# Performance work log

Hardware: AMD Instinct MI355X
Metric: run time of the kernel (lower is better)

The kernel has to match this reference:

```python
import jax, jax.numpy as jnp
import numpy as np


def setup_inputs() -> dict:
    key = jax.random.key(0)
    image = jax.random.randint(key, (4, 2048, 2048), 0, 50000, dtype=jnp.int32)
    return {"image": image}


def reference(image) -> jnp.ndarray:
    # Faithful, single-pass equivalent of LabelGapAdjustment(shift=False).
    # The original while-loop (decrement labels above each missing label until
    # labels are the consecutive set 1..K) is exactly dense-rank remapping:
    # new_label = 1-based rank of the label among the sorted unique labels.
    imin = image.min()
    image_shift = 1 - imin
    shifted = jnp.where(imin <= 0, image + image_shift, image)

    flat = shifted.reshape(-1)
    order = jnp.argsort(flat)
    s = flat[order]  # sorted labels
    # 1 where a new distinct value starts; cumsum -> 1-based dense rank
    is_new = jnp.concatenate(
        [jnp.ones((1,), dtype=jnp.int32), (s[1:] != s[:-1]).astype(jnp.int32)]
    )
    ranks_sorted = jnp.cumsum(is_new)  # [N], values 1..K
    # scatter ranks back to original positions
    ranks = jnp.zeros_like(flat).at[order].set(ranks_sorted.astype(flat.dtype))
    compact = ranks.reshape(image.shape)

    # shift=False: undo the shift (original subtracts image_shift unconditionally)
    return compact - image_shift
```

## Files before the change

### kernel.cpp

```cpp
#include <hip/hip_runtime.h>
#include <limits.h>

#define TABLE 65536
#define NBITW (TABLE / 32)
#define NTAB  512
#define CHUNK 16
#define MIN_OFF 0
#define BITS_OFF 64
#define PACK_OFF (64 + NBITW)
#define TAB_OFF  (PACK_OFF + 2 * NBITW)

__global__ __launch_bounds__(1024) void lga_mark_kernel(const int* __restrict__ img,
                                                        int n, int n4, int* ws) {
    __shared__ unsigned char tbl[TABLE];
    unsigned int* tbl32 = (unsigned int*)tbl;
    int t = threadIdx.x;
    for (int i = t; i < TABLE / 4; i += 1024) tbl32[i] = 0;
    if (blockIdx.x == 0) {
        for (int i = t; i < NBITW; i += 1024) ws[BITS_OFF + i] = 0;
    }
    __syncthreads();

    int stride = gridDim.x * blockDim.x;
    for (int i = blockIdx.x * blockDim.x + t; i < n4; i += stride) {
        int4 v = ((const int4*)img)[i];
        tbl[v.x] = 1;
        tbl[v.y] = 1;
        tbl[v.z] = 1;
        tbl[v.w] = 1;
    }
    if (blockIdx.x == 0 && t == 0) {
        for (int j = n4 * 4; j < n; ++j) tbl[img[j]] = 1;
    }
    __syncthreads();

    unsigned int* mytab = (unsigned int*)(ws + TAB_OFF) + blockIdx.x * NBITW;
    for (int d = t; d < NBITW; d += 1024) {
        const unsigned int* p = tbl32 + d * 8;
        unsigned int m = 0;
        #pragma unroll
        for (int j = 0; j < 8; ++j) {
            unsigned int w = p[j];
            m |= (w & 1u) << (j * 4);
            m |= ((w >> 8) & 1u) << (j * 4 + 1);
            m |= ((w >> 16) & 1u) << (j * 4 + 2);
            m |= ((w >> 24) & 1u) << (j * 4 + 3);
        }
        mytab[d] = m;
    }
}

__global__ __launch_bounds__(128) void lga_merge_kernel(int* ws) {
    int d = blockIdx.x * 128 + threadIdx.x;
    const unsigned int* tabs = (const unsigned int*)(ws + TAB_OFF)
                             + (size_t)blockIdx.y * CHUNK * NBITW;
    unsigned int m = 0;
    #pragma unroll
    for (int k = 0; k < CHUNK; ++k) m |= tabs[k * NBITW + d];
    if (m) atomicOr((unsigned int*)(ws + BITS_OFF) + d, m);
}

__global__ __launch_bounds__(1024) void lga_scan_kernel(int* ws) {
    const unsigned int* bits = (const unsigned int*)(ws + BITS_OFF);
    uint4* pack = (uint4*)(ws + PACK_OFF);
    int t = threadIdx.x;
    int lane = t & 63;
    int wave = t >> 6;

    unsigned int d0 = bits[2 * t], d1 = bits[2 * t + 1];
    int c0 = __popc(d0);
    int s = c0 + __popc(d1);
    int firstset;
    if (d0)      firstset = 64 * t + __ffs(d0) - 1;
    else if (d1) firstset = 64 * t + 32 + __ffs(d1) - 1;
    else         firstset = INT_MAX;

    int v = s;
    #pragma unroll
    for (int off = 1; off < 64; off <<= 1) {
        int u = __shfl_up(v, off, 64);
        if (lane >= off) v += u;
    }
    int fm = firstset;
    #pragma unroll
    for (int off = 32; off > 0; off >>= 1)
        fm = min(fm, __shfl_down(fm, off, 64));

    __shared__ int wsum[16];
    __shared__ int wmin[16];
    if (lane == 63) wsum[wave] = v;
    if (lane == 0)  wmin[wave] = fm;
    __syncthreads();
    if (wave == 0 && lane < 16) {
        int w = wsum[lane];
        #pragma unroll
        for (int off = 1; off < 16; off <<= 1) {
            int u = __shfl_up(w, off, 16);
            if (lane >= off) w += u;
        }
        wsum[lane] = w;
        int m = wmin[lane];
        #pragma unroll
        for (int off = 8; off > 0; off >>= 1)
            m = min(m, __shfl_down(m, off, 16));
        if (lane == 0) ws[MIN_OFF] = m;
    }
    __syncthreads();

    unsigned int excl = (unsigned int)(v - s + (wave > 0 ? wsum[wave - 1] : 0));
    pack[t] = make_uint4(excl, d0, excl + (unsigned int)c0, d1);
}

__global__ __launch_bounds__(1024) void lga_remap_kernel(const int* __restrict__ img,
                                                         int* __restrict__ out,
                                                         int n, int n4,
                                                         const int* __restrict__ ws) {
    __shared__ uint2 lp[NBITW];
    const uint2* pack = (const uint2*)(ws + PACK_OFF);
    int t = threadIdx.x;
    for (int i = t; i < NBITW; i += 1024) lp[i] = pack[i];
    int imin = ws[MIN_OFF];
    __syncthreads();

    int stride = gridDim.x * blockDim.x;
    for (int i = blockIdx.x * blockDim.x + t; i < n4; i += stride) {
        int4 v = ((const int4*)img)[i];
        int4 r;
        {
            uint2 p = lp[((unsigned)v.x) >> 5];
            r.x = (int)(p.x + __popc(p.y & ((1u << (v.x & 31)) - 1u))) + imin;
        }
        {
            uint2 p = lp[((unsigned)v.y) >> 5];
            r.y = (int)(p.x + __popc(p.y & ((1u << (v.y & 31)) - 1u))) + imin;
        }
        {
            uint2 p = lp[((unsigned)v.z) >> 5];
            r.z = (int)(p.x + __popc(p.y & ((1u << (v.z & 31)) - 1u))) + imin;
        }
        {
            uint2 p = lp[((unsigned)v.w) >> 5];
            r.w = (int)(p.x + __popc(p.y & ((1u << (v.w & 31)) - 1u))) + imin;
        }
        ((int4*)out)[i] = r;
    }
    if (blockIdx.x == 0 && t == 0) {
        for (int j = n4 * 4; j < n; ++j) {
            unsigned v = (unsigned)img[j];
            uint2 p = lp[v >> 5];
            out[j] = (int)(p.x + __popc(p.y & ((1u << (v & 31)) - 1u))) + imin;
        }
    }
}

extern "C" void kernel_launch(void* const* d_in, const int* in_sizes, int n_in,
                              void* d_out, int out_size, void* d_ws, size_t ws_size,
                              hipStream_t stream) {
    const int* img = (const int*)d_in[0];
    int* out = (int*)d_out;
    int* ws = (int*)d_ws;
    int n = in_sizes[0];
    int n4 = n / 4;

    lga_mark_kernel<<<NTAB, 1024, 0, stream>>>(img, n, n4, ws);
    lga_merge_kernel<<<dim3(NBITW / 128, NTAB / CHUNK), 128, 0, stream>>>(ws);
    lga_scan_kernel<<<1, 1024, 0, stream>>>(ws);
    lga_remap_kernel<<<512, 1024, 0, stream>>>(img, out, n, n4, ws);
}
```

Baseline: 127.3 us.

## Fuse merge and scan kernels via last-block atomic counter, fold min into ranks

New measurement: 141.3 us. 11.0% more time.

```diff
diff --git a/kernel.cpp b/kernel.cpp
--- a/kernel.cpp
+++ b/kernel.cpp
@@ -6,6 +6,7 @@
 #define NTAB  512
 #define CHUNK 16
 #define MIN_OFF 0
+#define CNT_OFF 8
 #define BITS_OFF 64
 #define PACK_OFF (64 + NBITW)
 #define TAB_OFF  (PACK_OFF + 2 * NBITW)
@@ -18,6 +19,7 @@
     for (int i = t; i < TABLE / 4; i += 1024) tbl32[i] = 0;
     if (blockIdx.x == 0) {
         for (int i = t; i < NBITW; i += 1024) ws[BITS_OFF + i] = 0;
+        if (t == 0) ws[CNT_OFF] = 0;
     }
     __syncthreads();
 
@@ -50,31 +52,42 @@
     }
 }
 
-__global__ __launch_bounds__(128) void lga_merge_kernel(int* ws) {
-    int d = blockIdx.x * 128 + threadIdx.x;
+__global__ __launch_bounds__(256) void lga_merge_scan_kernel(int* ws) {
+    int t = threadIdx.x;
+    int d = blockIdx.x * 256 + t;
     const unsigned int* tabs = (const unsigned int*)(ws + TAB_OFF)
                              + (size_t)blockIdx.y * CHUNK * NBITW;
     unsigned int m = 0;
     #pragma unroll
     for (int k = 0; k < CHUNK; ++k) m |= tabs[k * NBITW + d];
     if (m) atomicOr((unsigned int*)(ws + BITS_OFF) + d, m);
-}
+    __threadfence();
+    __shared__ int lastFlag;
+    __syncthreads();
+    if (t == 0) {
+        int prev = atomicAdd(ws + CNT_OFF, 1);
+        lastFlag = (prev == (int)(gridDim.x * gridDim.y) - 1);
+    }
+    __syncthreads();
+    if (!lastFlag) return;
 
-__global__ __launch_bounds__(1024) void lga_scan_kernel(int* ws) {
-    const unsigned int* bits = (const unsigned int*)(ws + BITS_OFF);
-    uint4* pack = (uint4*)(ws + PACK_OFF);
-    int t = threadIdx.x;
-    int lane = t & 63;
-    int wave = t >> 6;
+    unsigned int* bitsp = (unsigned int*)(ws + BITS_OFF);
+    unsigned int w[8];
+    int c[8];
+    int s = 0;
+    #pragma unroll
+    for (int j = 0; j < 8; ++j) {
+        w[j] = __hip_atomic_load(bitsp + 8 * t + j, __ATOMIC_RELAXED,
+                                 __HIP_MEMORY_SCOPE_AGENT);
+        c[j] = __popc(w[j]);
+        s += c[j];
+    }
+    int firstset = INT_MAX;
+    #pragma unroll
+    for (int j = 7; j >= 0; --j)
+        if (w[j]) firstset = 32 * (8 * t + j) + __ffs(w[j]) - 1;
 
-    unsigned int d0 = bits[2 * t], d1 = bits[2 * t + 1];
-    int c0 = __popc(d0);
-    int s = c0 + __popc(d1);
-    int firstset;
-    if (d0)      firstset = 64 * t + __ffs(d0) - 1;
-    else if (d1) firstset = 64 * t + 32 + __ffs(d1) - 1;
-    else         firstset = INT_MAX;
-
+    int lane = t & 63, wave = t >> 6;
     int v = s;
     #pragma unroll
     for (int off = 1; off < 64; off <<= 1) {
@@ -86,40 +99,34 @@
     for (int off = 32; off > 0; off >>= 1)
         fm = min(fm, __shfl_down(fm, off, 64));
 
-    __shared__ int wsum[16];
-    __shared__ int wmin[16];
+    __shared__ int wsum[4];
+    __shared__ int wmin[4];
     if (lane == 63) wsum[wave] = v;
     if (lane == 0)  wmin[wave] = fm;
     __syncthreads();
-    if (wave == 0 && lane < 16) {
-        int w = wsum[lane];
-        #pragma unroll
-        for (int off = 1; off < 16; off <<= 1) {
-            int u = __shfl_up(w, off, 16);
-            if (lane >= off) w += u;
-        }
-        wsum[lane] = w;
-        int m = wmin[lane];
-        #pragma unroll
-        for (int off = 8; off > 0; off >>= 1)
-            m = min(m, __shfl_down(m, off, 16));
-        if (lane == 0) ws[MIN_OFF] = m;
+    int imin = min(min(wmin[0], wmin[1]), min(wmin[2], wmin[3]));
+    if (t == 0) ws[MIN_OFF] = imin;
+    int base = 0;
+    if (wave > 0) base += wsum[0];
+    if (wave > 1) base += wsum[1];
+    if (wave > 2) base += wsum[2];
+    unsigned int excl = (unsigned int)(base + (v - s) + imin);
+    uint2* pack = (uint2*)(ws + PACK_OFF);
+    #pragma unroll
+    for (int j = 0; j < 8; ++j) {
+        pack[8 * t + j] = make_uint2(excl, w[j]);
+        excl += (unsigned int)c[j];
     }
-    __syncthreads();
-
-    unsigned int excl = (unsigned int)(v - s + (wave > 0 ? wsum[wave - 1] : 0));
-    pack[t] = make_uint4(excl, d0, excl + (unsigned int)c0, d1);
 }
 
 __global__ __launch_bounds__(1024) void lga_remap_kernel(const int* __restrict__ img,
                                                          int* __restrict__ out,
                                                          int n, int n4,
                                                          const int* __restrict__ ws) {
-    __shared__ uint2 lp[NBITW];
-    const uint2* pack = (const uint2*)(ws + PACK_OFF);
+    __shared__ __align__(16) uint2 lp[NBITW];
+    const uint4* pack4 = (const uint4*)(ws + PACK_OFF);
     int t = threadIdx.x;
-    for (int i = t; i < NBITW; i += 1024) lp[i] = pack[i];
-    int imin = ws[MIN_OFF];
+    for (int i = t; i < NBITW / 2; i += 1024) ((uint4*)lp)[i] = pack4[i];
     __syncthreads();
 
     int stride = gridDim.x * blockDim.x;
@@ -128,19 +135,19 @@
         int4 r;
         {
             uint2 p = lp[((unsigned)v.x) >> 5];
-            r.x = (int)(p.x + __popc(p.y & ((1u << (v.x & 31)) - 1u))) + imin;
+            r.x = (int)(p.x + __popc(p.y & ((1u << (v.x & 31)) - 1u)));
         }
         {
             uint2 p = lp[((unsigned)v.y) >> 5];
-            r.y = (int)(p.x + __popc(p.y & ((1u << (v.y & 31)) - 1u))) + imin;
+            r.y = (int)(p.x + __popc(p.y & ((1u << (v.y & 31)) - 1u)));
         }
         {
             uint2 p = lp[((unsigned)v.z) >> 5];
-            r.z = (int)(p.x + __popc(p.y & ((1u << (v.z & 31)) - 1u))) + imin;
+            r.z = (int)(p.x + __popc(p.y & ((1u << (v.z & 31)) - 1u)));
         }
         {
             uint2 p = lp[((unsigned)v.w) >> 5];
-            r.w = (int)(p.x + __popc(p.y & ((1u << (v.w & 31)) - 1u))) + imin;
+            r.w = (int)(p.x + __popc(p.y & ((1u << (v.w & 31)) - 1u)));
         }
         ((int4*)out)[i] = r;
     }
@@ -148,7 +155,7 @@
         for (int j = n4 * 4; j < n; ++j) {
             unsigned v = (unsigned)img[j];
             uint2 p = lp[v >> 5];
-            out[j] = (int)(p.x + __popc(p.y & ((1u << (v & 31)) - 1u))) + imin;
+            out[j] = (int)(p.x + __popc(p.y & ((1u << (v & 31)) - 1u)));
         }
     }
 }
@@ -163,7 +170,6 @@
     int n4 = n / 4;
 
     lga_mark_kernel<<<NTAB, 1024, 0, stream>>>(img, n, n4, ws);
-    lga_merge_kernel<<<dim3(NBITW / 128, NTAB / CHUNK), 128, 0, stream>>>(ws);
-    lga_scan_kernel<<<1, 1024, 0, stream>>>(ws);
+    lga_merge_scan_kernel<<<dim3(NBITW / 256, NTAB / CHUNK), 256, 0, stream>>>(ws);
     lga_remap_kernel<<<512, 1024, 0, stream>>>(img, out, n, n4, ws);
 }
```
